# Kernel optimization log

Hardware: AMD Instinct MI355X
Metric: run time of the kernel (lower is better)

The kernel has to match this reference:

```python
import jax, jax.numpy as jnp
import numpy as np

N = 50000      # nodes
E = 800000     # edges
F_IN = 128     # input_channels
H = 128        # hidden_channels
OUT = 10       # output_channels
G = 64         # graphs in batch


def setup_inputs() -> dict:
    key = jax.random.key(0)
    ks = jax.random.split(key, 16)
    s = 0.05
    inp = {
        "x": jax.random.normal(ks[0], (N, F_IN), jnp.float32),
        "edge_index": jax.random.randint(ks[1], (2, E), 0, N, jnp.int64 if jax.config.jax_enable_x64 else jnp.int32),
        "batch": jnp.sort(jax.random.randint(ks[2], (N,), 0, G, jnp.int32)),
        "conv1_w": jax.random.normal(ks[3], (F_IN, H), jnp.float32) * s,
        "conv1_b": jnp.zeros((H,), jnp.float32),
        "conv2_w": jax.random.normal(ks[4], (H, H), jnp.float32) * s,
        "conv2_b": jnp.zeros((H,), jnp.float32),
        "conv3_w": jax.random.normal(ks[5], (H, H), jnp.float32) * s,
        "conv3_b": jnp.zeros((H,), jnp.float32),
        "fc1_w": jax.random.normal(ks[6], (H, 8 * H), jnp.float32) * s,
        "fc1_b": jnp.zeros((8 * H,), jnp.float32),
        "fc2_w": jax.random.normal(ks[7], (8 * H, 4 * H), jnp.float32) * s,
        "fc2_b": jnp.zeros((4 * H,), jnp.float32),
        "fc3_w": jax.random.normal(ks[8], (4 * H, 2 * H), jnp.float32) * s,
        "fc3_b": jnp.zeros((2 * H,), jnp.float32),
        "fc4_w": jax.random.normal(ks[9], (2 * H, H), jnp.float32) * s,
        "fc4_b": jnp.zeros((H,), jnp.float32),
        "fc5_w": jax.random.normal(ks[10], (H, OUT), jnp.float32) * s,
        "fc5_b": jnp.zeros((OUT,), jnp.float32),
    }
    return inp


def _gcn_conv(x, w, b, src, dst, norm, n_nodes):
    # GCNConv: out = D^{-1/2} (A + I) D^{-1/2} X W + b   (self-loops already in src/dst)
    xw = x @ w                                        # [N, H]
    msg = xw[src] * norm[:, None]                     # gather + scale, [E+N, H]
    return jax.ops.segment_sum(msg, dst, num_segments=n_nodes) + b


def reference(x, edge_index, batch,
              conv1_w, conv1_b, conv2_w, conv2_b, conv3_w, conv3_b,
              fc1_w, fc1_b, fc2_w, fc2_b, fc3_w, fc3_b,
              fc4_w, fc4_b, fc5_w, fc5_b):
    n = x.shape[0]
    loop = jnp.arange(n, dtype=edge_index.dtype)
    src = jnp.concatenate([edge_index[0], loop])      # add self-loops
    dst = jnp.concatenate([edge_index[1], loop])
    deg = jax.ops.segment_sum(jnp.ones_like(dst, dtype=x.dtype), dst, num_segments=n)
    dinv = jnp.where(deg > 0, jax.lax.rsqrt(deg), 0.0)
    norm = dinv[src] * dinv[dst]                      # symmetric normalization per edge

    h = jax.nn.relu(_gcn_conv(x, conv1_w, conv1_b, src, dst, norm, n))
    h = jax.nn.relu(_gcn_conv(h, conv2_w, conv2_b, src, dst, norm, n))
    h = _gcn_conv(h, conv3_w, conv3_b, src, dst, norm, n)

    # global mean pool over graphs
    sums = jax.ops.segment_sum(h, batch, num_segments=G)
    cnt = jax.ops.segment_sum(jnp.ones((n,), x.dtype), batch, num_segments=G)
    f = sums / jnp.maximum(cnt, 1.0)[:, None]         # [G, H]

    y = jax.nn.relu(f @ fc1_w + fc1_b)
    y = jax.nn.relu(y @ fc2_w + fc2_b)
    y = jax.nn.relu(y @ fc3_w + fc3_b)
    y = jax.nn.relu(y @ fc4_w + fc4_b)
    # dropout p=0.5 is identity in eval mode
    y = y @ fc5_w + fc5_b                             # [G, OUT]
    return (f, y)
```

## Files before the change

### kernel.cpp

```cpp
#include <hip/hip_runtime.h>
#include <stdint.h>

#define N_NODES 50000
#define N_EDGES 800000
#define N_PAD   50176
#define PCHUNK  512
#define NCHUNKS 98
#define FEAT    128
#define NGRAPH  64

#define E_BLKS      3125
#define GSTRIP_BLKS 782
#define GR_BLKS     (GSTRIP_BLKS + E_BLKS)
#define CZ_BLKS     3136
#define AGG_BLKS    12500

typedef __attribute__((ext_vector_type(8))) short short8;
typedef __attribute__((ext_vector_type(4))) float floatx4;

static __device__ __forceinline__ ushort f2bf(float f) {
  uint32_t x = __float_as_uint(f);
  x += 0x7FFF + ((x >> 16) & 1);
  return (ushort)(x >> 16);
}
static __device__ __forceinline__ float bfLo(uint32_t u) {
  return __uint_as_float(u << 16);
}
static __device__ __forceinline__ float bfHi(uint32_t u) {
  return __uint_as_float(u & 0xFFFF0000u);
}

static __device__ __forceinline__ void cvt4T(const float* __restrict__ in,
                                             ushort* __restrict__ outT, int i) {
  float4 v = ((const float4*)in)[i];
  int k = (4 * i) >> 7;
  int n = (4 * i) & 127;
  outT[(size_t)(n + 0) * FEAT + k] = f2bf(v.x);
  outT[(size_t)(n + 1) * FEAT + k] = f2bf(v.y);
  outT[(size_t)(n + 2) * FEAT + k] = f2bf(v.z);
  outT[(size_t)(n + 3) * FEAT + k] = f2bf(v.w);
}

__global__ __launch_bounds__(256) void wcvt(const float* __restrict__ w0,
                                            const float* __restrict__ w1,
                                            ushort* __restrict__ wbT,
                                            float* __restrict__ coefT) {
  int b = blockIdx.x, t = threadIdx.x;
  if (b < 32) {
    int i = b * 256 + t;
    if (i < 4096) cvt4T(w0, wbT, i);
    else cvt4T(w1, wbT + FEAT * FEAT, i - 4096);
  } else {
    int i = (b - 32) * 256 + t;
    ((float4*)coefT)[i] = make_float4(0.f, 0.f, 0.f, 0.f);
  }
}

static __device__ __forceinline__ void gemm_strip_f32a(int strip, int lane,
                                                       const float* __restrict__ X,
                                                       const ushort* __restrict__ WT,
                                                       ushort* __restrict__ XW) {
  if (strip >= N_NODES / 16) return;
  int m0 = strip * 16;
  int r = lane & 15, quad = lane >> 4;
  const float* xrow = X + (size_t)(m0 + r) * FEAT;
  short8 afr[4];
#pragma unroll
  for (int kb = 0; kb < 4; ++kb) {
    int k0 = kb * 32 + quad * 8;
    float4 f0 = *(const float4*)(xrow + k0);
    float4 f1 = *(const float4*)(xrow + k0 + 4);
    short8 a;
    a[0] = (short)f2bf(f0.x); a[1] = (short)f2bf(f0.y);
    a[2] = (short)f2bf(f0.z); a[3] = (short)f2bf(f0.w);
    a[4] = (short)f2bf(f1.x); a[5] = (short)f2bf(f1.y);
    a[6] = (short)f2bf(f1.z); a[7] = (short)f2bf(f1.w);
    afr[kb] = a;
  }
#pragma unroll
  for (int nt = 0; nt < 8; ++nt) {
    int n0 = nt * 16;
    floatx4 acc = {0.f, 0.f, 0.f, 0.f};
    const ushort* wrow = WT + (size_t)(n0 + r) * FEAT;
#pragma unroll
    for (int kb = 0; kb < 4; ++kb) {
      short8 b = *(const short8*)(wrow + kb * 32 + quad * 8);
      acc = __builtin_amdgcn_mfma_f32_16x16x32_bf16(afr[kb], b, acc, 0, 0, 0);
    }
#pragma unroll
    for (int reg = 0; reg < 4; ++reg)
      XW[(size_t)(m0 + quad * 4 + reg) * FEAT + n0 + r] = f2bf(acc[reg]);
  }
}

__global__ __launch_bounds__(256) void gemm_rank(const float* __restrict__ x,
                                                 const ushort* __restrict__ wbT,
                                                 ushort* __restrict__ msl,
                                                 const int* __restrict__ dst,
                                                 int* __restrict__ cnt_p,
                                                 int* __restrict__ rank) {
  int b = blockIdx.x, t = threadIdx.x;
  int fifth = b / 5;
  if (b - fifth * 5 == 0) {
    gemm_strip_f32a(fifth * 4 + (t >> 6), t & 63, x, wbT, msl);
  } else {
    int e = (b - fifth - 1) * 256 + t;
    rank[e] = atomicAdd(&cnt_p[dst[e] * 8], 1);
  }
}

__global__ __launch_bounds__(256) void gemm2_strip(const ushort* __restrict__ X,
                                                   const ushort* __restrict__ WT,
                                                   ushort* __restrict__ XW) {
  int strip = (blockIdx.x * 256 + threadIdx.x) >> 6;
  int lane = threadIdx.x & 63;
  if (strip >= N_NODES / 16) return;
  int m0 = strip * 16;
  int r = lane & 15, quad = lane >> 4;
  const ushort* xrow = X + (size_t)(m0 + r) * FEAT;
  short8 afr[4];
#pragma unroll
  for (int kb = 0; kb < 4; ++kb)
    afr[kb] = *(const short8*)(xrow + kb * 32 + quad * 8);
#pragma unroll
  for (int nt = 0; nt < 8; ++nt) {
    int n0 = nt * 16;
    floatx4 acc = {0.f, 0.f, 0.f, 0.f};
    const ushort* wrow = WT + (size_t)(n0 + r) * FEAT;
#pragma unroll
    for (int kb = 0; kb < 4; ++kb) {
      short8 b = *(const short8*)(wrow + kb * 32 + quad * 8);
      acc = __builtin_amdgcn_mfma_f32_16x16x32_bf16(afr[kb], b, acc, 0, 0, 0);
    }
#pragma unroll
    for (int reg = 0; reg < 4; ++reg)
      XW[(size_t)(m0 + quad * 4 + reg) * FEAT + n0 + r] = f2bf(acc[reg]);
  }
}

__global__ __launch_bounds__(256) void dinv_scan1(const int* __restrict__ cnt_p,
                                                  const int* __restrict__ batch,
                                                  float* __restrict__ dinv,
                                                  float* __restrict__ cnt_g,
                                                  int* __restrict__ ptr,
                                                  int* __restrict__ bsums,
                                                  float* __restrict__ coefT) {
  __shared__ int tmp[256];
  __shared__ int bins[NGRAPH];
  if (threadIdx.x < NGRAPH) bins[threadIdx.x] = 0;
  int i = blockIdx.x * 256 + threadIdx.x;
  int v = (i < N_NODES) ? cnt_p[i * 8] : 0;
  tmp[threadIdx.x] = v;
  __syncthreads();
  for (int off = 1; off < 256; off <<= 1) {
    int t = (threadIdx.x >= off) ? tmp[threadIdx.x - off] : 0;
    __syncthreads();
    tmp[threadIdx.x] += t;
    __syncthreads();
  }
  if (i < N_NODES) ptr[i] = tmp[threadIdx.x] - v;
  if (threadIdx.x == 255) bsums[blockIdx.x] = tmp[255];
  if (i < N_NODES) {
    float di = rsqrtf((float)v + 1.0f);
    dinv[i] = di;
    int g = batch[i];
    coefT[(size_t)g * N_PAD + i] = di * di;
    atomicAdd(&bins[g], 1);
  }
  __syncthreads();
  if (threadIdx.x < NGRAPH && bins[threadIdx.x] > 0)
    atomicAdd(&cnt_g[threadIdx.x], (float)bins[threadIdx.x]);
}

__global__ __launch_bounds__(256) void scan2(int* __restrict__ bsums, int nb) {
  __shared__ int tmp[256];
  int v = (threadIdx.x < nb) ? bsums[threadIdx.x] : 0;
  tmp[threadIdx.x] = v;
  __syncthreads();
  for (int off = 1; off < 256; off <<= 1) {
    int t = (threadIdx.x >= off) ? tmp[threadIdx.x - off] : 0;
    __syncthreads();
    tmp[threadIdx.x] += t;
    __syncthreads();
  }
  if (threadIdx.x < nb) bsums[threadIdx.x] = tmp[threadIdx.x] - v;
}

__global__ __launch_bounds__(256) void scan3(int* __restrict__ ptr,
                                             const int* __restrict__ bsums) {
  int i = blockIdx.x * 256 + threadIdx.x;
  if (i < N_NODES) ptr[i] += bsums[blockIdx.x];
}

__global__ __launch_bounds__(256) void fill_csr(const int* __restrict__ src,
                                                const int* __restrict__ dst,
                                                const int* __restrict__ rank,
                                                const int* __restrict__ ptr,
                                                const float* __restrict__ dinv,
                                                int2* __restrict__ edges) {
  int e = blockIdx.x * 256 + threadIdx.x;
  if (e >= N_EDGES) return;
  int s = src[e];
  edges[ptr[dst[e]] + rank[e]] = make_int2(s, __float_as_int(dinv[s]));
}

static __device__ __forceinline__ float2 agg_node(const uint32_t* __restrict__ m32,
                                                  const int2* __restrict__ edges,
                                                  int start, int n, int lane) {
  float ax0 = 0.f, ay0 = 0.f, ax1 = 0.f, ay1 = 0.f;
  float ax2 = 0.f, ay2 = 0.f, ax3 = 0.f, ay3 = 0.f;
  int i = 0;
  if ((start & 1) && n > 0) {
    int2 e = edges[start];
    uint32_t u = m32[(size_t)e.x * 64 + lane];
    float nrm = __int_as_float(e.y);
    ax0 = fmaf(nrm, bfLo(u), ax0);
    ay0 = fmaf(nrm, bfHi(u), ay0);
    i = 1;
  }
  for (; i + 8 <= n; i += 8) {
    const int4* ep = (const int4*)(edges + start + i);
    int4 q0 = ep[0], q1 = ep[1], q2 = ep[2], q3 = ep[3];
    uint32_t u0 = m32[(size_t)q0.x * 64 + lane];
    uint32_t u1 = m32[(size_t)q0.z * 64 + lane];
    uint32_t u2 = m32[(size_t)q1.x * 64 + lane];
    uint32_t u3 = m32[(size_t)q1.z * 64 + lane];
    uint32_t u4 = m32[(size_t)q2.x * 64 + lane];
    uint32_t u5 = m32[(size_t)q2.z * 64 + lane];
    uint32_t u6 = m32[(size_t)q3.x * 64 + lane];
    uint32_t u7 = m32[(size_t)q3.z * 64 + lane];
    float n0 = __int_as_float(q0.y), n1 = __int_as_float(q0.w);
    float n2 = __int_as_float(q1.y), n3 = __int_as_float(q1.w);
    float n4 = __int_as_float(q2.y), n5 = __int_as_float(q2.w);
    float n6 = __int_as_float(q3.y), n7 = __int_as_float(q3.w);
    ax0 = fmaf(n0, bfLo(u0), ax0); ay0 = fmaf(n0, bfHi(u0), ay0);
    ax1 = fmaf(n1, bfLo(u1), ax1); ay1 = fmaf(n1, bfHi(u1), ay1);
    ax2 = fmaf(n2, bfLo(u2), ax2); ay2 = fmaf(n2, bfHi(u2), ay2);
    ax3 = fmaf(n3, bfLo(u3), ax3); ay3 = fmaf(n3, bfHi(u3), ay3);
    ax0 = fmaf(n4, bfLo(u4), ax0); ay0 = fmaf(n4, bfHi(u4), ay0);
    ax1 = fmaf(n5, bfLo(u5), ax1); ay1 = fmaf(n5, bfHi(u5), ay1);
    ax2 = fmaf(n6, bfLo(u6), ax2); ay2 = fmaf(n6, bfHi(u6), ay2);
    ax3 = fmaf(n7, bfLo(u7), ax3); ay3 = fmaf(n7, bfHi(u7), ay3);
  }
  for (; i < n; ++i) {
    int2 e = edges[start + i];
    float nrm = __int_as_float(e.y);
    uint32_t u = m32[(size_t)e.x * 64 + lane];
    ax0 = fmaf(nrm, bfLo(u), ax0);
    ay0 = fmaf(nrm, bfHi(u), ay0);
  }
  return make_float2((ax0 + ax1) + (ax2 + ax3), (ay0 + ay1) + (ay2 + ay3));
}

static __device__ __forceinline__ void agg_one(int v, int lane,
                                               const ushort* __restrict__ msg,
                                               const float* __restrict__ dinv,
                                               const int* __restrict__ ptr,
                                               const int* __restrict__ cnt_p,
                                               const int2* __restrict__ edges,
                                               const float* __restrict__ bias,
                                               ushort* __restrict__ outp) {
  float di = dinv[v];
  const uint32_t* m32 = (const uint32_t*)msg;
  uint32_t su = m32[(size_t)v * 64 + lane];
  float2 s = agg_node(m32, edges, ptr[v], cnt_p[v * 8], lane);
  float ax = fmaf(fmaf(di, bfLo(su), s.x), di, bias[2 * lane]);
  float ay = fmaf(fmaf(di, bfHi(su), s.y), di, bias[2 * lane + 1]);
  ushort2 h2;
  h2.x = f2bf(fmaxf(ax, 0.f));
  h2.y = f2bf(fmaxf(ay, 0.f));
  ((ushort2*)outp)[(size_t)v * 64 + lane] = h2;
}

__global__ __launch_bounds__(256) void agg1_coef(const ushort* __restrict__ msg,
                                                 const float* __restrict__ dinv,
                                                 const int* __restrict__ ptr,
                                                 const int* __restrict__ cnt_p,
                                                 const int2* __restrict__ edges,
                                                 const float* __restrict__ bias,
                                                 ushort* __restrict__ outp,
                                                 const int* __restrict__ src,
                                                 const int* __restrict__ dst,
                                                 const int* __restrict__ batch,
                                                 float* __restrict__ coefT) {
  int b = blockIdx.x, t = threadIdx.x;
  int fifth = b / 5;
  int rem = b - fifth * 5;
  if (rem < 4) {
    int ab = fifth * 4 + rem;
    agg_one(ab * 4 + (t >> 6), t & 63, msg, dinv, ptr, cnt_p, edges, bias, outp);
  } else {
    int e = fifth * 256 + t;
    int s = src[e], d = dst[e];
    atomicAdd(&coefT[(size_t)batch[d] * N_PAD + s], dinv[s] * dinv[d]);
  }
}

__global__ __launch_bounds__(256) void agg_kernel(const ushort* __restrict__ msg,
                                                  const float* __restrict__ dinv,
                                                  const int* __restrict__ ptr,
                                                  const int* __restrict__ cnt_p,
                                                  const int2* __restrict__ edges,
                                                  const float* __restrict__ bias,
                                                  ushort* __restrict__ outp) {
  int wave = (blockIdx.x * 256 + threadIdx.x) >> 6;
  if (wave >= N_NODES) return;
  agg_one(wave, threadIdx.x & 63, msg, dinv, ptr, cnt_p, edges, bias, outp);
}

__global__ __launch_bounds__(512) void pool_mfma(const ushort* __restrict__ h2,
                                                 const float* __restrict__ coefT,
                                                 float* __restrict__ P) {
  __shared__ ushort cs[64 * PCHUNK];
  int t = threadIdx.x;
  int lane = t & 63;
  int w = t >> 6;
  int r = lane & 15, quad = lane >> 4;
  int n0 = w * 16;
  floatx4 acc[4];
#pragma unroll
  for (int mt = 0; mt < 4; ++mt) acc[mt] = (floatx4){0.f, 0.f, 0.f, 0.f};
#pragma unroll 1
  for (int cc = 0; cc < 2; ++cc) {
    int c0 = (blockIdx.x * 2 + cc) * PCHUNK;
#pragma unroll 4
    for (int it = 0; it < 16; ++it) {
      int f4 = t + it * 512;
      int g = f4 >> 7;
      int k = (f4 & 127) * 4;
      float4 v = *(const float4*)(coefT + (size_t)g * N_PAD + c0 + k);
      ushort4 u;
      u.x = f2bf(v.x); u.y = f2bf(v.y); u.z = f2bf(v.z); u.w = f2bf(v.w);
      uint32_t off = ((uint32_t)g * (PCHUNK * 2) + k * 2) ^ ((g & 7) << 4);
      *(ushort4*)((char*)cs + off) = u;
    }
    __syncthreads();
#pragma unroll 2
    for (int kb = 0; kb < 16; ++kb) {
      int k0c = kb * 32 + quad * 8;
      short8 bfr;
#pragma unroll
      for (int j = 0; j < 8; ++j)
        bfr[j] = (short)h2[(size_t)(c0 + k0c + j) * FEAT + n0 + r];
#pragma unroll
      for (int mt = 0; mt < 4; ++mt) {
        int row = mt * 16 + r;
        uint32_t off = ((uint32_t)row * (PCHUNK * 2) + k0c * 2) ^ ((row & 7) << 4);
        short8 a = *(const short8*)((const char*)cs + off);
        acc[mt] = __builtin_amdgcn_mfma_f32_16x16x32_bf16(a, bfr, acc[mt], 0, 0, 0);
      }
    }
    __syncthreads();
  }
#pragma unroll
  for (int mt = 0; mt < 4; ++mt)
#pragma unroll
    for (int reg = 0; reg < 4; ++reg)
      atomicAdd(&P[(size_t)(mt * 16 + quad * 4 + reg) * FEAT + n0 + r],
                acc[mt][reg]);
}

template <int K, int C, int KSLICE, int RELU_IN, int DIVC, int NSPLIT>
__global__ __launch_bounds__(256) void fc_layer(const float* __restrict__ IN,
                                                const float* __restrict__ W,
                                                const float* __restrict__ Bs,
                                                const float* __restrict__ cntg,
                                                float* __restrict__ OUT) {
  constexpr int CB = (C + 63) / 64;
  int lane = threadIdx.x & 63;
  int gq = threadIdx.x >> 6;
  int bid = blockIdx.x;
  int kp = bid % NSPLIT;
  int rest = bid / NSPLIT;
  int cg = rest % CB;
  int g = (rest / CB) * 4 + gq;
  int c = cg * 64 + lane;
  if (c >= C) return;
  int k0 = kp * KSLICE;
  const float* wp = W + (size_t)k0 * C + c;
  const float* in = IN + (size_t)g * K + k0;
  float cf = 1.f;
  if (DIVC) cf = fmaxf(cntg[g], 1.f);
  float a0 = 0.f, a1 = 0.f, a2 = 0.f, a3 = 0.f;
  float a4 = 0.f, a5 = 0.f, a6 = 0.f, a7 = 0.f;
#pragma unroll 2
  for (int k = 0; k < KSLICE; k += 8) {
    float i0 = in[k + 0], i1 = in[k + 1], i2 = in[k + 2], i3 = in[k + 3];
    float i4 = in[k + 4], i5 = in[k + 5], i6 = in[k + 6], i7 = in[k + 7];
    if (RELU_IN) {
      i0 = fmaxf(i0, 0.f); i1 = fmaxf(i1, 0.f);
      i2 = fmaxf(i2, 0.f); i3 = fmaxf(i3, 0.f);
      i4 = fmaxf(i4, 0.f); i5 = fmaxf(i5, 0.f);
      i6 = fmaxf(i6, 0.f); i7 = fmaxf(i7, 0.f);
    }
    if (DIVC) {
      i0 /= cf; i1 /= cf; i2 /= cf; i3 /= cf;
      i4 /= cf; i5 /= cf; i6 /= cf; i7 /= cf;
    }
    a0 = fmaf(i0, wp[(size_t)(k + 0) * C], a0);
    a1 = fmaf(i1, wp[(size_t)(k + 1) * C], a1);
    a2 = fmaf(i2, wp[(size_t)(k + 2) * C], a2);
    a3 = fmaf(i3, wp[(size_t)(k + 3) * C], a3);
    a4 = fmaf(i4, wp[(size_t)(k + 4) * C], a4);
    a5 = fmaf(i5, wp[(size_t)(k + 5) * C], a5);
    a6 = fmaf(i6, wp[(size_t)(k + 6) * C], a6);
    a7 = fmaf(i7, wp[(size_t)(k + 7) * C], a7);
  }
  float s = ((a0 + a1) + (a2 + a3)) + ((a4 + a5) + (a6 + a7));
  if (NSPLIT == 1) {
    OUT[(size_t)g * C + c] = s + Bs[c];
  } else {
    atomicAdd(&OUT[(size_t)g * C + c], s + (kp == 0 ? Bs[c] : 0.f));
  }
}

extern "C" void kernel_launch(void* const* d_in, const int* in_sizes, int n_in,
                              void* d_out, int out_size, void* d_ws, size_t ws_size,
                              hipStream_t stream) {
  const float* x         = (const float*)d_in[0];
  const int*   ei        = (const int*)d_in[1];
  const int*   batch     = (const int*)d_in[2];
  const float* conv_w[3] = {(const float*)d_in[3], (const float*)d_in[5], (const float*)d_in[7]};
  const float* conv_b[3] = {(const float*)d_in[4], (const float*)d_in[6], (const float*)d_in[8]};
  const float* fc_w[5]   = {(const float*)d_in[9],  (const float*)d_in[11],
                            (const float*)d_in[13], (const float*)d_in[15],
                            (const float*)d_in[17]};
  const float* fc_b[5]   = {(const float*)d_in[10], (const float*)d_in[12],
                            (const float*)d_in[14], (const float*)d_in[16],
                            (const float*)d_in[18]};
  const int* e_src = ei;
  const int* e_dst = ei + N_EDGES;
  float* out_f = (float*)d_out;
  float* out_y = (float*)d_out + NGRAPH * FEAT;

  char* p = (char*)d_ws;
  auto carve = [&](size_t bytes) {
    char* r = p;
    p += (bytes + 255) & ~(size_t)255;
    return r;
  };
  int*    cnt_p   = (int*)carve((size_t)N_NODES * 32);
  float*  dinv    = (float*)carve(N_NODES * 4);
  int*    csr_ptr = (int*)carve(N_NODES * 4);
  int*    bsums   = (int*)carve(256 * 4);
  int2*   edges   = (int2*)carve((size_t)N_EDGES * 8);
  ushort* wbT     = (ushort*)carve((size_t)2 * FEAT * FEAT * 2);
  ushort* hbuf    = (ushort*)carve((size_t)N_PAD * FEAT * 2);
  float*  coefT   = (float*)carve((size_t)NGRAPH * N_PAD * 4);
  float*  f_sum   = (float*)carve(NGRAPH * FEAT * 4);
  float*  cnt_g   = (float*)carve(NGRAPH * 4);
  float*  Y1      = (float*)carve(NGRAPH * 1024 * 4);
  float*  Y2      = (float*)carve(NGRAPH * 512 * 4);
  float*  Y3      = (float*)carve(NGRAPH * 256 * 4);
  float*  Y4      = (float*)carve(NGRAPH * 128 * 4);
  char*   region  = carve((size_t)N_EDGES * 4 + (size_t)N_NODES * FEAT * 2);
  int*    rank    = (int*)region;
  ushort* msl1    = (ushort*)(region + (size_t)N_EDGES * 4);
  ushort* msl2    = (ushort*)region;

  const int BLK_N = (N_NODES + 255) / 256;

  hipMemsetAsync(cnt_p, 0, (size_t)N_NODES * 32, stream);
  hipMemsetAsync(f_sum, 0, NGRAPH * FEAT * 4 + 256, stream);
  hipMemsetAsync(Y2, 0, NGRAPH * (512 + 256 + 128) * 4, stream);

  wcvt<<<32 + CZ_BLKS, 256, 0, stream>>>(conv_w[0], conv_w[1], wbT, coefT);

  gemm_rank<<<GR_BLKS, 256, 0, stream>>>(x, wbT, msl1, e_dst, cnt_p, rank);

  dinv_scan1<<<BLK_N, 256, 0, stream>>>(cnt_p, batch, dinv, cnt_g, csr_ptr,
                                        bsums, coefT);
  scan2<<<1, 256, 0, stream>>>(bsums, BLK_N);
  scan3<<<BLK_N, 256, 0, stream>>>(csr_ptr, bsums);

  fill_csr<<<E_BLKS, 256, 0, stream>>>(e_src, e_dst, rank, csr_ptr, dinv, edges);

  agg1_coef<<<AGG_BLKS + E_BLKS, 256, 0, stream>>>(
      msl1, dinv, csr_ptr, cnt_p, edges, conv_b[0], hbuf,
      e_src, e_dst, batch, coefT);
  gemm2_strip<<<GSTRIP_BLKS, 256, 0, stream>>>(hbuf, wbT + FEAT * FEAT, msl2);
  agg_kernel<<<(N_NODES + 3) / 4, 256, 0, stream>>>(msl2, dinv, csr_ptr, cnt_p,
                                                    edges, conv_b[1], hbuf);
  pool_mfma<<<NCHUNKS / 2, 512, 0, stream>>>(hbuf, coefT, f_sum);

  fc_layer< 128, 128, 128, 0, 1, 1><<< 32, 256, 0, stream>>>(f_sum, conv_w[2], conv_b[2], cnt_g, out_f);
  fc_layer< 128,1024, 128, 0, 0, 1><<<256, 256, 0, stream>>>(out_f, fc_w[0], fc_b[0], nullptr, Y1);
  fc_layer<1024, 512, 256, 1, 0, 4><<<512, 256, 0, stream>>>(Y1, fc_w[1], fc_b[1], nullptr, Y2);
  fc_layer< 512, 256, 128, 1, 0, 4><<<256, 256, 0, stream>>>(Y2, fc_w[2], fc_b[2], nullptr, Y3);
  fc_layer< 256, 128,  32, 1, 0, 8><<<256, 256, 0, stream>>>(Y3, fc_w[3], fc_b[3], nullptr, Y4);
  fc_layer< 128,  10, 128, 1, 0, 1><<< 16, 256, 0, stream>>>(Y4, fc_w[4], fc_b[4], nullptr, out_y);
}
```

Measured before the change: 348.3 us.

## Split coef scatter across both aggregation passes, fold scan3 into consumers

The coefficient-scatter work for the pooling matrix is now split in half, and each half is interleaved with one of the two aggregation kernels (8 aggregation blocks per scatter block) instead of all of it riding on the first pass. The scan3 launch is removed: consumers add the block prefix from bsums on the fly in fill_csr and agg_one. Degree counters are padded to 128-byte stride to reduce atomic contention on shared cache lines. The agg_node tail gains 4-wide and 2-wide unrolled steps to cut scalar remainder iterations. The trade-off is larger counter memset and extra per-access bsums loads.

Measured after the change: 337.1 us. 3.2% less time.

```diff
diff --git a/kernel.cpp b/kernel.cpp
--- a/kernel.cpp
+++ b/kernel.cpp
@@ -13,7 +13,8 @@
 #define GSTRIP_BLKS 782
 #define GR_BLKS     (GSTRIP_BLKS + E_BLKS)
 #define CZ_BLKS     3136
-#define AGG_BLKS    12500
+#define E1_SPLIT    399872
+#define AGGC_GRID   (1563 * 9)
 
 typedef __attribute__((ext_vector_type(8))) short short8;
 typedef __attribute__((ext_vector_type(4))) float floatx4;
@@ -105,7 +106,7 @@
     gemm_strip_f32a(fifth * 4 + (t >> 6), t & 63, x, wbT, msl);
   } else {
     int e = (b - fifth - 1) * 256 + t;
-    rank[e] = atomicAdd(&cnt_p[dst[e] * 8], 1);
+    rank[e] = atomicAdd(&cnt_p[dst[e] * 32], 1);
   }
 }
 
@@ -149,7 +150,7 @@
   __shared__ int bins[NGRAPH];
   if (threadIdx.x < NGRAPH) bins[threadIdx.x] = 0;
   int i = blockIdx.x * 256 + threadIdx.x;
-  int v = (i < N_NODES) ? cnt_p[i * 8] : 0;
+  int v = (i < N_NODES) ? cnt_p[i * 32] : 0;
   tmp[threadIdx.x] = v;
   __syncthreads();
   for (int off = 1; off < 256; off <<= 1) {
@@ -186,22 +187,18 @@
   if (threadIdx.x < nb) bsums[threadIdx.x] = tmp[threadIdx.x] - v;
 }
 
-__global__ __launch_bounds__(256) void scan3(int* __restrict__ ptr,
-                                             const int* __restrict__ bsums) {
-  int i = blockIdx.x * 256 + threadIdx.x;
-  if (i < N_NODES) ptr[i] += bsums[blockIdx.x];
-}
-
 __global__ __launch_bounds__(256) void fill_csr(const int* __restrict__ src,
                                                 const int* __restrict__ dst,
                                                 const int* __restrict__ rank,
                                                 const int* __restrict__ ptr,
+                                                const int* __restrict__ bsums,
                                                 const float* __restrict__ dinv,
                                                 int2* __restrict__ edges) {
   int e = blockIdx.x * 256 + threadIdx.x;
   if (e >= N_EDGES) return;
   int s = src[e];
-  edges[ptr[dst[e]] + rank[e]] = make_int2(s, __float_as_int(dinv[s]));
+  int d = dst[e];
+  edges[ptr[d] + bsums[d >> 8] + rank[e]] = make_int2(s, __float_as_int(dinv[s]));
 }
 
 static __device__ __forceinline__ float2 agg_node(const uint32_t* __restrict__ m32,
@@ -242,6 +239,31 @@
     ax2 = fmaf(n6, bfLo(u6), ax2); ay2 = fmaf(n6, bfHi(u6), ay2);
     ax3 = fmaf(n7, bfLo(u7), ax3); ay3 = fmaf(n7, bfHi(u7), ay3);
   }
+  if (i + 4 <= n) {
+    const int4* ep = (const int4*)(edges + start + i);
+    int4 q0 = ep[0], q1 = ep[1];
+    uint32_t u0 = m32[(size_t)q0.x * 64 + lane];
+    uint32_t u1 = m32[(size_t)q0.z * 64 + lane];
+    uint32_t u2 = m32[(size_t)q1.x * 64 + lane];
+    uint32_t u3 = m32[(size_t)q1.z * 64 + lane];
+    float n0 = __int_as_float(q0.y), n1 = __int_as_float(q0.w);
+    float n2 = __int_as_float(q1.y), n3 = __int_as_float(q1.w);
+    ax0 = fmaf(n0, bfLo(u0), ax0); ay0 = fmaf(n0, bfHi(u0), ay0);
+    ax1 = fmaf(n1, bfLo(u1), ax1); ay1 = fmaf(n1, bfHi(u1), ay1);
+    ax2 = fmaf(n2, bfLo(u2), ax2); ay2 = fmaf(n2, bfHi(u2), ay2);
+    ax3 = fmaf(n3, bfLo(u3), ax3); ay3 = fmaf(n3, bfHi(u3), ay3);
+    i += 4;
+  }
+  if (i + 2 <= n) {
+    const int4* ep = (const int4*)(edges + start + i);
+    int4 q0 = ep[0];
+    uint32_t u0 = m32[(size_t)q0.x * 64 + lane];
+    uint32_t u1 = m32[(size_t)q0.z * 64 + lane];
+    float n0 = __int_as_float(q0.y), n1 = __int_as_float(q0.w);
+    ax0 = fmaf(n0, bfLo(u0), ax0); ay0 = fmaf(n0, bfHi(u0), ay0);
+    ax1 = fmaf(n1, bfLo(u1), ax1); ay1 = fmaf(n1, bfHi(u1), ay1);
+    i += 2;
+  }
   for (; i < n; ++i) {
     int2 e = edges[start + i];
     float nrm = __int_as_float(e.y);
@@ -256,6 +278,7 @@
                                                const ushort* __restrict__ msg,
                                                const float* __restrict__ dinv,
                                                const int* __restrict__ ptr,
+                                               const int* __restrict__ bsums,
                                                const int* __restrict__ cnt_p,
                                                const int2* __restrict__ edges,
                                                const float* __restrict__ bias,
@@ -263,7 +286,8 @@
   float di = dinv[v];
   const uint32_t* m32 = (const uint32_t*)msg;
   uint32_t su = m32[(size_t)v * 64 + lane];
-  float2 s = agg_node(m32, edges, ptr[v], cnt_p[v * 8], lane);
+  int start = ptr[v] + bsums[v >> 8];
+  float2 s = agg_node(m32, edges, start, cnt_p[v * 32], lane);
   float ax = fmaf(fmaf(di, bfLo(su), s.x), di, bias[2 * lane]);
   float ay = fmaf(fmaf(di, bfHi(su), s.y), di, bias[2 * lane + 1]);
   ushort2 h2;
@@ -272,40 +296,34 @@
   ((ushort2*)outp)[(size_t)v * 64 + lane] = h2;
 }
 
-__global__ __launch_bounds__(256) void agg1_coef(const ushort* __restrict__ msg,
-                                                 const float* __restrict__ dinv,
-                                                 const int* __restrict__ ptr,
-                                                 const int* __restrict__ cnt_p,
-                                                 const int2* __restrict__ edges,
-                                                 const float* __restrict__ bias,
-                                                 ushort* __restrict__ outp,
-                                                 const int* __restrict__ src,
-                                                 const int* __restrict__ dst,
-                                                 const int* __restrict__ batch,
-                                                 float* __restrict__ coefT) {
+template <int PHASE>
+__global__ __launch_bounds__(256) void agg_coef(const ushort* __restrict__ msg,
+                                                const float* __restrict__ dinv,
+                                                const int* __restrict__ ptr,
+                                                const int* __restrict__ bsums,
+                                                const int* __restrict__ cnt_p,
+                                                const int2* __restrict__ edges,
+                                                const float* __restrict__ bias,
+                                                ushort* __restrict__ outp,
+                                                const int* __restrict__ src,
+                                                const int* __restrict__ dst,
+                                                const int* __restrict__ batch,
+                                                float* __restrict__ coefT) {
   int b = blockIdx.x, t = threadIdx.x;
-  int fifth = b / 5;
-  int rem = b - fifth * 5;
-  if (rem < 4) {
-    int ab = fifth * 4 + rem;
-    agg_one(ab * 4 + (t >> 6), t & 63, msg, dinv, ptr, cnt_p, edges, bias, outp);
+  int grp = b / 9;
+  int rem = b - grp * 9;
+  if (rem < 8) {
+    int ab = grp * 8 + rem;
+    if (ab >= 12500) return;
+    agg_one(ab * 4 + (t >> 6), t & 63, msg, dinv, ptr, bsums, cnt_p, edges,
+            bias, outp);
   } else {
-    int e = fifth * 256 + t;
-    int s = src[e], d = dst[e];
-    atomicAdd(&coefT[(size_t)batch[d] * N_PAD + s], dinv[s] * dinv[d]);
-  }
-}
-
-__global__ __launch_bounds__(256) void agg_kernel(const ushort* __restrict__ msg,
-                                                  const float* __restrict__ dinv,
-                                                  const int* __restrict__ ptr,
-                                                  const int* __restrict__ cnt_p,
-                                                  const int2* __restrict__ edges,
-                                                  const float* __restrict__ bias,
-                                                  ushort* __restrict__ outp) {
-  int wave = (blockIdx.x * 256 + threadIdx.x) >> 6;
-  if (wave >= N_NODES) return;
-  agg_one(wave, threadIdx.x & 63, msg, dinv, ptr, cnt_p, edges, bias, outp);
+    int e = (PHASE ? E1_SPLIT : 0) + grp * 256 + t;
+    if (e < (PHASE ? N_EDGES : E1_SPLIT)) {
+      int s = src[e], d = dst[e];
+      atomicAdd(&coefT[(size_t)batch[d] * N_PAD + s], dinv[s] * dinv[d]);
+    }
+  }
 }
 
 __global__ __launch_bounds__(512) void pool_mfma(const ushort* __restrict__ h2,
@@ -439,7 +457,7 @@
     p += (bytes + 255) & ~(size_t)255;
     return r;
   };
-  int*    cnt_p   = (int*)carve((size_t)N_NODES * 32);
+  int*    cnt_p   = (int*)carve((size_t)N_NODES * 128);
   float*  dinv    = (float*)carve(N_NODES * 4);
   int*    csr_ptr = (int*)carve(N_NODES * 4);
   int*    bsums   = (int*)carve(256 * 4);
@@ -460,7 +478,7 @@
 
   const int BLK_N = (N_NODES + 255) / 256;
 
-  hipMemsetAsync(cnt_p, 0, (size_t)N_NODES * 32, stream);
+  hipMemsetAsync(cnt_p, 0, (size_t)N_NODES * 128, stream);
   hipMemsetAsync(f_sum, 0, NGRAPH * FEAT * 4 + 256, stream);
   hipMemsetAsync(Y2, 0, NGRAPH * (512 + 256 + 128) * 4, stream);
 
@@ -471,16 +489,17 @@
   dinv_scan1<<<BLK_N, 256, 0, stream>>>(cnt_p, batch, dinv, cnt_g, csr_ptr,
                                         bsums, coefT);
   scan2<<<1, 256, 0, stream>>>(bsums, BLK_N);
-  scan3<<<BLK_N, 256, 0, stream>>>(csr_ptr, bsums);
-
-  fill_csr<<<E_BLKS, 256, 0, stream>>>(e_src, e_dst, rank, csr_ptr, dinv, edges);
-
-  agg1_coef<<<AGG_BLKS + E_BLKS, 256, 0, stream>>>(
-      msl1, dinv, csr_ptr, cnt_p, edges, conv_b[0], hbuf,
+
+  fill_csr<<<E_BLKS, 256, 0, stream>>>(e_src, e_dst, rank, csr_ptr, bsums,
+                                       dinv, edges);
+
+  agg_coef<0><<<AGGC_GRID, 256, 0, stream>>>(
+      msl1, dinv, csr_ptr, bsums, cnt_p, edges, conv_b[0], hbuf,
       e_src, e_dst, batch, coefT);
   gemm2_strip<<<GSTRIP_BLKS, 256, 0, stream>>>(hbuf, wbT + FEAT * FEAT, msl2);
-  agg_kernel<<<(N_NODES + 3) / 4, 256, 0, stream>>>(msl2, dinv, csr_ptr, cnt_p,
-                                                    edges, conv_b[1], hbuf);
+  agg_coef<1><<<AGGC_GRID, 256, 0, stream>>>(
+      msl2, dinv, csr_ptr, bsums, cnt_p, edges, conv_b[1], hbuf,
+      e_src, e_dst, batch, coefT);
   pool_mfma<<<NCHUNKS / 2, 512, 0, stream>>>(hbuf, coefT, f_sum);
 
   fc_layer< 128, 128, 128, 0, 1, 1><<< 32, 256, 0, stream>>>(f_sum, conv_w[2], conv_b[2], cnt_g, out_f);
```
